# Performance work log

Measured on AMD Instinct MI355X. Metric: run time of the kernel, lower is better.

Reference implementation:

```python
import jax, jax.numpy as jnp
import numpy as np

# ---- module config (mirrors arch_args / init_kwargs) ----
W_BITS_PER_SLICE = 4      # slice_init=True -> weights quantized with STE to w_bits_per_slice
A_BITS = 8                # activation quantization bits
A_BITS_PER_STREAM = 8
VMAX = 1.0
GON_HW, GOFF_HW = 1.0, 1e-3   # weight_to_diff_conductance is called with Gon=1, Goff=1/1000 (hardcoded)
ADC_PREC = 8
ADC_STEP = 1e-3           # adc_static_step
NUM_SUBARRAYS = 9
SUB_SIZE = 256            # subarray_size; 256*3*3 / 256 = 9 even chunks
K, STRIDE, PAD = 3, 1, 1


def ste_quantize(x, bits):
    # Symmetric uniform quantizer with straight-through estimator (STE_Quantize).
    n = float(2 ** bits - 1)
    s = jnp.max(jnp.abs(x)) + 1e-12
    q = jnp.round(x / s * n) / n * s
    return x + jax.lax.stop_gradient(q - x)


def adc_quantize(I):
    # Nbit_ADC: static-step uniform ADC, signed (adc_pos_only=False), deterministic
    # rounding (adc_stoch_round=False), STE backward, no custom loss.
    half = 2 ** (ADC_PREC - 1)
    q = jnp.clip(jnp.round(I / ADC_STEP), -half, half - 1) * ADC_STEP
    return I + jax.lax.stop_gradient(q - I)


def setup_inputs():
    key = jax.random.key(0)
    k1, k2 = jax.random.split(key)
    x = jax.random.normal(k1, (32, 256, 32, 32), jnp.float32)
    fan_in = 256 * K * K
    w = jax.random.normal(k2, (256, 256, K, K), jnp.float32) * np.sqrt(2.0 / fan_in)  # kaiming_normal
    return {"inputs": x, "weight": w}


def reference(inputs, weight):
    B = inputs.shape[0]
    O = weight.shape[0]

    # forward(): quantize activations (a_bits) and weights (w_bits_per_slice, slice_init path)
    qa = ste_quantize(inputs, A_BITS)
    qw = ste_quantize(weight, W_BITS_PER_SLICE)

    # F.unfold -> [B, C*k*k, L], channel-major patch ordering (matches torch)
    patches = jax.lax.conv_general_dilated_patches(
        qa, (K, K), (STRIDE, STRIDE), ((PAD, PAD), (PAD, PAD)))
    Hp, Wp = patches.shape[2], patches.shape[3]
    L = Hp * Wp
    V = patches.reshape(B, NUM_SUBARRAYS, SUB_SIZE, L) * (VMAX / A_BITS_PER_STREAM)

    # Differential conductances: G_pos - G_neg. The dummy columns (both filled with
    # Goff) cancel exactly in I_pos - I_neg, so the net current per subarray is a
    # single contraction against qw * (Gon - Goff) / Nstates_slice.
    nstates = float(2 ** W_BITS_PER_SLICE - 1)
    Gd = qw.reshape(O, NUM_SUBARRAYS, SUB_SIZE) * ((GON_HW - GOFF_HW) / nstates)

    # per-subarray crossbar currents: [B, n_sub, O, L]
    I = jnp.einsum('bgfl,ogf->bgol', V, Gd)

    # shared ADC applied to each subarray output, then accumulate over subarrays
    accum = adc_quantize(I).sum(axis=1)  # [B, O, L]
    a_loss = jnp.float32(0.0)            # adc_custom_loss=False

    # F.fold with (1,1) kernel onto sqrt(L) x sqrt(L) grid == reshape
    result = accum.reshape(B, O, Hp, Wp)
    return (result, a_loss)
```

## Files before the change

kernel.cpp:

```cpp
#include <hip/hip_runtime.h>
#include <stdint.h>

typedef unsigned short u16;
typedef __attribute__((ext_vector_type(8))) short short8;
typedef __attribute__((ext_vector_type(4))) short s4v;
typedef __attribute__((ext_vector_type(4))) float floatx4;

#define NB 32
#define NC 256
#define NH 32
#define NW 32
#define NO 256
#define NPIX (NH*NW)
#define KPIX 9
#define NG 9
#define RUN 32
#define GK (NG*RUN)
#define KTOT (NG*GK)
#define PADH 34
#define PADSP (PADH*PADH)
#define QA_BSTRIDE (PADSP*NC)
#define CHS 40

#define AS1 __attribute__((address_space(1)))
#define AS3 __attribute__((address_space(3)))

__global__ void fused_pre(const float4* __restrict__ x4, int nx4,
                          const float4* __restrict__ w4, int nw4,
                          float* __restrict__ pmax, u16* __restrict__ qa) {
  int bid = blockIdx.x;
  if (bid >= 1088) {
    int zb = bid - 1088;
    int b = zb / 9;
    int rem = (zb % 9) * 256 + threadIdx.x;
    if (rem >= 2112) return;
    int pb = rem >> 4, c16 = rem & 15;
    int y, x;
    if (pb < 68) { y = (pb >= 34) ? 33 : 0; x = pb % 34; }
    else { int q = pb - 68; y = 1 + (q >> 1); x = (q & 1) ? 33 : 0; }
    uint4 z; z.x = z.y = z.z = z.w = 0u;
    *(uint4*)(qa + ((size_t)(b * PADH + y) * PADH + x) * NC + c16 * 16) = z;
    return;
  }
  const float4* p; int n4; int nb, b0;
  if (bid < 1024) { p = x4; n4 = nx4; nb = 1024; b0 = bid; }
  else            { p = w4; n4 = nw4; nb = 64;   b0 = bid - 1024; }
  float m = 0.f;
  for (int i = b0 * blockDim.x + threadIdx.x; i < n4; i += nb * blockDim.x) {
    float4 v = p[i];
    m = fmaxf(m, fmaxf(fmaxf(fabsf(v.x), fabsf(v.y)), fmaxf(fabsf(v.z), fabsf(v.w))));
  }
#pragma unroll
  for (int off = 32; off > 0; off >>= 1)
    m = fmaxf(m, __shfl_down(m, off, 64));
  __shared__ float sm[4];
  int lane = threadIdx.x & 63, wv = threadIdx.x >> 6;
  if (lane == 0) sm[wv] = m;
  __syncthreads();
  if (threadIdx.x == 0)
    pmax[bid] = fmaxf(fmaxf(sm[0], sm[1]), fmaxf(sm[2], sm[3]));
}

__device__ inline void reduce_pmax(const float* pmax, int tid, int nthreads,
                                   float* sred, float& mx_out, float& mw_out) {
  const float4* pf4 = (const float4*)pmax;
  float mx = 0.f, mw = 0.f;
  for (int t = tid; t < 256; t += nthreads) {
    float4 v = pf4[t];
    mx = fmaxf(mx, fmaxf(fmaxf(v.x, v.y), fmaxf(v.z, v.w)));
  }
  if (tid < 16) {
    float4 v = pf4[256 + tid];
    mw = fmaxf(fmaxf(v.x, v.y), fmaxf(v.z, v.w));
  }
#pragma unroll
  for (int off = 32; off > 0; off >>= 1) {
    mx = fmaxf(mx, __shfl_down(mx, off, 64));
    mw = fmaxf(mw, __shfl_down(mw, off, 64));
  }
  int lane = tid & 63, wv = tid >> 6, nw = nthreads >> 6;
  if (lane == 0) { sred[wv] = mx; sred[8 + wv] = mw; }
  __syncthreads();
  mx = sred[0]; mw = sred[8];
  for (int i = 1; i < nw; i++) { mx = fmaxf(mx, sred[i]); mw = fmaxf(mw, sred[8 + i]); }
  mx_out = mx; mw_out = mw;
}

__global__ void fused_quant(const float* __restrict__ x, const float* __restrict__ w,
                            const float* __restrict__ pmax,
                            u16* __restrict__ qa, u16* __restrict__ wq,
                            float* __restrict__ lossp) {
  __shared__ float sred[16];
  float mx, mw;
  reduce_pmax(pmax, threadIdx.x, 256, sred, mx, mw);
  int bid = blockIdx.x, tid = threadIdx.x;
  if (bid < 1024) {
    __shared__ u16 ts[32][264];
    double s = (double)mx + 1e-12;
    double inv = 255.0 / s;
    int b = bid >> 5, y = bid & 31;
    const float4* x4 = (const float4*)x;
    int xc = tid & 7, crow = tid >> 3;
#pragma unroll
    for (int it = 0; it < 8; it++) {
      int c = crow + 32 * it;
      float4 v = x4[((size_t)(b * NC + c) * NH + y) * 8 + xc];
      float q0 = (float)rint((double)v.x * inv);
      float q1 = (float)rint((double)v.y * inv);
      float q2 = (float)rint((double)v.z * inv);
      float q3 = (float)rint((double)v.w * inv);
      ts[xc * 4 + 0][c] = (u16)(__float_as_uint(q0) >> 16);
      ts[xc * 4 + 1][c] = (u16)(__float_as_uint(q1) >> 16);
      ts[xc * 4 + 2][c] = (u16)(__float_as_uint(q2) >> 16);
      ts[xc * 4 + 3][c] = (u16)(__float_as_uint(q3) >> 16);
    }
    __syncthreads();
    int xx = tid >> 3, qwl = tid & 7;
    u16* orow = qa + ((size_t)(b * PADH + y + 1) * PADH + (xx + 1)) * NC;
#pragma unroll
    for (int it = 0; it < 4; it++) {
      int qw = qwl + 8 * it;
      *(uint4*)(orow + qw * 8) = *(const uint4*)&ts[xx][qw * 8];
    }
    return;
  }
  double s = (double)mw + 1e-12;
  double inv = 15.0 / s;
  int idx = (bid - 1024) * 256 + tid;
  if (idx == 0) *lossp = 0.0f;
  int o = idx / KTOT, kk = idx % KTOT;
  int g = kk / GK, rem = kk % GK;
  int r = rem / RUN, j = rem % RUN;
  int clo = (256 * g - r + 8) / 9;
  int chi = (256 * (g + 1) - r + 8) / 9; if (chi > NC) chi = NC;
  int cst = clo & ~3;
  int c = cst + j;
  float val = 0.f;
  if (c >= clo && c < chi) {
    float wv = w[((size_t)o * NC + c) * KPIX + r];
    val = (float)rint((double)wv * inv);
  }
  wq[idx] = (u16)(__float_as_uint(val) >> 16);
}

__global__ __launch_bounds__(256, 2) void gemm_adc(const u16* __restrict__ qa,
                                                   const u16* __restrict__ wq,
                                                   const float* __restrict__ pmax,
                                                   float* __restrict__ out) {
  __shared__ u16 sA[8192];
  __shared__ u16 lB[3 * 128 * RUN];
  __shared__ float sred[16];
  const int tid = threadIdx.x;
  float mx, mw;
  reduce_pmax(pmax, tid, 256, sred, mx, mw);

  const int mblk = blockIdx.x, nblk = blockIdx.y;
  const int b = mblk >> 3;
  const int p0 = (mblk & 7) * 128;
  const int y0 = (mblk & 7) * 4;
  const int n0 = nblk * 128;
  const int lane = tid & 63, wv = tid >> 6;
  const int wm = (wv & 1) * 64, wn = (wv >> 1) * 64;
  const int fm = lane & 15, fq = lane >> 4;
  const int swz = (fq + ((fm >> 1) & 3)) & 3;
  const int fq8 = fq * 8;

  double sa = (double)mx + 1e-12;
  double sw = (double)mw + 1e-12;
  double Sstep = sa * sw * 0.999 / 459.0;

  int pix40[4];
#pragma unroll
  for (int mi = 0; mi < 4; mi++) {
    int pr = wm + mi * 16 + fm;
    pix40[mi] = ((pr >> 5) * 34 + (pr & 31)) * CHS;
  }

  const int r0 = tid >> 2;
  const int jsrc = ((tid & 3) - ((tid >> 3) & 3)) & 3;
  const u16* BbH[2];
#pragma unroll
  for (int h = 0; h < 2; h++)
    BbH[h] = wq + (size_t)(n0 + r0 + 64 * h) * KTOT + jsrc * 8;

  const u16* Abase = qa + (size_t)b * QA_BSTRIDE + (size_t)y0 * PADH * NC;

  floatx4 acc[4][4];
  float tot[4][4][4];
#pragma unroll
  for (int mi = 0; mi < 4; mi++)
#pragma unroll
    for (int ni = 0; ni < 4; ni++)
#pragma unroll
      for (int rr = 0; rr < 4; rr++) { acc[mi][ni][rr] = 0.f; tot[mi][ni][rr] = 0.f; }

#pragma unroll 1
  for (int g = 0; g < NG; g++) {
    int cw = ((256 * g) / 9) & ~3;
#pragma unroll 1
    for (int rc = 0; rc < 3; rc++) {
      int kb[3], dA[3];
#pragma unroll
      for (int ri = 0; ri < 3; ri++) {
        int r = rc * 3 + ri;
        int cst = ((256 * g - r + 8) / 9) & ~3;
        dA[ri] = cst - cw;
        kb[ri] = g * GK + r * RUN;
      }
      if (rc == 0) {
        const u16* src = Abase + cw;
#pragma unroll
        for (int i = 0; i < 4; i++) {
          int s = tid + 256 * i;
          int py = s / 170;
          int rem = s - py * 170;
          int px = rem / 5;
          int j = rem - px * 5;
          __builtin_amdgcn_global_load_lds(
              (const AS1 void*)(src + (py * PADH + px) * NC + j * 8),
              (AS3 void*)&sA[s * 8], 16, 0, 0);
        }
      }
#pragma unroll
      for (int i = 0; i < 6; i++)
        __builtin_amdgcn_global_load_lds(
            (const AS1 void*)(BbH[i & 1] + kb[i >> 1]),
            (AS3 void*)&lB[(tid + 256 * i) * 8], 16, 0, 0);
      __syncthreads();
#pragma unroll
      for (int ri = 0; ri < 3; ri++) {
        short8 afr[4], bfr[4];
        int po = rc * (34 * CHS) + ri * CHS + dA[ri] + fq8;
        if (dA[ri] == 0) {
#pragma unroll
          for (int mi = 0; mi < 4; mi++)
            afr[mi] = *(const short8*)&sA[pix40[mi] + po];
        } else {
#pragma unroll
          for (int mi = 0; mi < 4; mi++) {
            union { short8 v8; s4v v4[2]; } u;
            u.v4[0] = *(const s4v*)&sA[pix40[mi] + po];
            u.v4[1] = *(const s4v*)&sA[pix40[mi] + po + 4];
            afr[mi] = u.v8;
          }
        }
#pragma unroll
        for (int ni = 0; ni < 4; ni++)
          bfr[ni] = *(const short8*)&lB[ri * 4096 + (wn + ni * 16 + fm) * RUN + swz * 8];
#pragma unroll
        for (int mi = 0; mi < 4; mi++)
#pragma unroll
          for (int ni = 0; ni < 4; ni++)
            acc[mi][ni] = __builtin_amdgcn_mfma_f32_16x16x32_bf16(afr[mi], bfr[ni], acc[mi][ni], 0, 0, 0);
      }
      __syncthreads();
    }
#pragma unroll
    for (int mi = 0; mi < 4; mi++)
#pragma unroll
      for (int ni = 0; ni < 4; ni++)
#pragma unroll
        for (int rr = 0; rr < 4; rr++) {
          double d = (double)acc[mi][ni][rr] * Sstep;
          float tf = (float)rint(d);
          tf = fminf(fmaxf(tf, -128.f), 127.f);
          tot[mi][ni][rr] += tf;
          acc[mi][ni][rr] = 0.f;
        }
  }
#pragma unroll
  for (int mi = 0; mi < 4; mi++)
#pragma unroll
    for (int ni = 0; ni < 4; ni++) {
      int o = n0 + wn + ni * 16 + fm;
      int p = p0 + wm + mi * 16 + fq * 4;
      float4 o4;
      o4.x = tot[mi][ni][0] * 1e-3f;
      o4.y = tot[mi][ni][1] * 1e-3f;
      o4.z = tot[mi][ni][2] * 1e-3f;
      o4.w = tot[mi][ni][3] * 1e-3f;
      *(float4*)(out + ((size_t)(b * NO + o)) * NPIX + p) = o4;
    }
}

extern "C" void kernel_launch(void* const* d_in, const int* in_sizes, int n_in,
                              void* d_out, int out_size, void* d_ws, size_t ws_size,
                              hipStream_t stream) {
  const float* x = (const float*)d_in[0];
  const float* w = (const float*)d_in[1];
  float* out = (float*)d_out;

  float* pmax = (float*)d_ws;
  u16* qa = (u16*)((char*)d_ws + 8192);
  u16* wq = (u16*)((char*)d_ws + 8192 + 18939904 + 8192);

  fused_pre<<<1376, 256, 0, stream>>>((const float4*)x, (NB * NC * NH * NW) / 4,
                                      (const float4*)w, (NO * NC * KPIX) / 4,
                                      pmax, qa);
  fused_quant<<<1024 + 2592, 256, 0, stream>>>(x, w, pmax, qa, wq, out + (out_size - 1));
  gemm_adc<<<dim3(256, 2), 256, 0, stream>>>(qa, wq, pmax, out);
}
```

Measured before the change: 154.8 us.

## Double-buffer A slab and B tiles with prefetch, swizzled LDS layout

Restructures the GEMM main loop into a flat 27-step software pipeline. Both the weight tile (lB) and the activation slab (sA32/sA8) are double-buffered, and the next stage's loads are issued before computing on the current one. Partial vmcnt waits and raw s_barrier replace full __syncthreads so that global-to-LDS copies overlap the MFMA work. The activation slab moves to a 32-channel rotated (swizzled) layout plus a small 8-channel tail buffer to reduce LDS bank conflicts, and s_setprio is raised around the compute. LDS use roughly doubles, which may reduce occupancy below two blocks per CU, and the hand-counted waitcnts are fragile.

Result: no change. 156.6 us (+1.1%).

```diff
diff --git a/kernel.cpp b/kernel.cpp
--- a/kernel.cpp
+++ b/kernel.cpp
@@ -20,7 +20,6 @@
 #define PADH 34
 #define PADSP (PADH*PADH)
 #define QA_BSTRIDE (PADSP*NC)
-#define CHS 40
 
 #define AS1 __attribute__((address_space(1)))
 #define AS3 __attribute__((address_space(3)))
@@ -147,8 +146,9 @@
                                                    const u16* __restrict__ wq,
                                                    const float* __restrict__ pmax,
                                                    float* __restrict__ out) {
-  __shared__ u16 sA[8192];
-  __shared__ u16 lB[3 * 128 * RUN];
+  __shared__ __align__(16) u16 lB[24576];
+  __shared__ __align__(16) u16 sA32[13056];
+  __shared__ __align__(16) u16 sA8[1632];
   __shared__ float sred[16];
   const int tid = threadIdx.x;
   float mx, mw;
@@ -163,17 +163,16 @@
   const int wm = (wv & 1) * 64, wn = (wv >> 1) * 64;
   const int fm = lane & 15, fq = lane >> 4;
   const int swz = (fq + ((fm >> 1) & 3)) & 3;
-  const int fq8 = fq * 8;
 
   double sa = (double)mx + 1e-12;
   double sw = (double)mw + 1e-12;
   double Sstep = sa * sw * 0.999 / 459.0;
 
-  int pix40[4];
+  int pixb[4];
 #pragma unroll
   for (int mi = 0; mi < 4; mi++) {
     int pr = wm + mi * 16 + fm;
-    pix40[mi] = ((pr >> 5) * 34 + (pr & 31)) * CHS;
+    pixb[mi] = (pr >> 5) * 34 + (pr & 31);
   }
 
   const int r0 = tid >> 2;
@@ -194,67 +193,33 @@
 #pragma unroll
       for (int rr = 0; rr < 4; rr++) { acc[mi][ni][rr] = 0.f; tot[mi][ni][rr] = 0.f; }
 
-#pragma unroll 1
-  for (int g = 0; g < NG; g++) {
-    int cw = ((256 * g) / 9) & ~3;
-#pragma unroll 1
-    for (int rc = 0; rc < 3; rc++) {
-      int kb[3], dA[3];
-#pragma unroll
-      for (int ri = 0; ri < 3; ri++) {
-        int r = rc * 3 + ri;
-        int cst = ((256 * g - r + 8) / 9) & ~3;
-        dA[ri] = cst - cw;
-        kb[ri] = g * GK + r * RUN;
+  auto STAGE_B = [&](int gs, int rcs, int bB) {
+    int kb0 = gs * GK + rcs * 3 * RUN;
+#pragma unroll
+    for (int i = 0; i < 6; i++)
+      __builtin_amdgcn_global_load_lds(
+          (const AS1 void*)(BbH[i & 1] + kb0 + (i >> 1) * RUN),
+          (AS3 void*)&lB[bB + (tid + 256 * i) * 8], 16, 0, 0);
+  };
+  auto STAGE_SLAB = [&](int gp, int aB) {
+    int cw = ((256 * gp) / 9) & ~3;
+    const u16* src = Abase + cw;
+    if (tid < 204) {
+#pragma unroll
+      for (int i = 0; i < 4; i++) {
+        int s = i * 204 + tid;
+        int p = s >> 2;
+        int js = ((s & 3) - ((s >> 3) & 3)) & 3;
+        __builtin_amdgcn_global_load_lds(
+            (const AS1 void*)(src + p * NC + js * 8),
+            (AS3 void*)&sA32[aB + s * 8], 16, 0, 0);
       }
-      if (rc == 0) {
-        const u16* src = Abase + cw;
-#pragma unroll
-        for (int i = 0; i < 4; i++) {
-          int s = tid + 256 * i;
-          int py = s / 170;
-          int rem = s - py * 170;
-          int px = rem / 5;
-          int j = rem - px * 5;
-          __builtin_amdgcn_global_load_lds(
-              (const AS1 void*)(src + (py * PADH + px) * NC + j * 8),
-              (AS3 void*)&sA[s * 8], 16, 0, 0);
-        }
-      }
-#pragma unroll
-      for (int i = 0; i < 6; i++)
-        __builtin_amdgcn_global_load_lds(
-            (const AS1 void*)(BbH[i & 1] + kb[i >> 1]),
-            (AS3 void*)&lB[(tid + 256 * i) * 8], 16, 0, 0);
-      __syncthreads();
-#pragma unroll
-      for (int ri = 0; ri < 3; ri++) {
-        short8 afr[4], bfr[4];
-        int po = rc * (34 * CHS) + ri * CHS + dA[ri] + fq8;
-        if (dA[ri] == 0) {
-#pragma unroll
-          for (int mi = 0; mi < 4; mi++)
-            afr[mi] = *(const short8*)&sA[pix40[mi] + po];
-        } else {
-#pragma unroll
-          for (int mi = 0; mi < 4; mi++) {
-            union { short8 v8; s4v v4[2]; } u;
-            u.v4[0] = *(const s4v*)&sA[pix40[mi] + po];
-            u.v4[1] = *(const s4v*)&sA[pix40[mi] + po + 4];
-            afr[mi] = u.v8;
-          }
-        }
-#pragma unroll
-        for (int ni = 0; ni < 4; ni++)
-          bfr[ni] = *(const short8*)&lB[ri * 4096 + (wn + ni * 16 + fm) * RUN + swz * 8];
-#pragma unroll
-        for (int mi = 0; mi < 4; mi++)
-#pragma unroll
-          for (int ni = 0; ni < 4; ni++)
-            acc[mi][ni] = __builtin_amdgcn_mfma_f32_16x16x32_bf16(afr[mi], bfr[ni], acc[mi][ni], 0, 0, 0);
-      }
-      __syncthreads();
-    }
+      __builtin_amdgcn_global_load_lds(
+          (const AS1 void*)(src + tid * NC + 32),
+          (AS3 void*)&sA8[tid * 8], 16, 0, 0);
+    }
+  };
+  auto FOLD = [&]() {
 #pragma unroll
     for (int mi = 0; mi < 4; mi++)
 #pragma unroll
@@ -267,13 +232,81 @@
           tot[mi][ni][rr] += tf;
           acc[mi][ni][rr] = 0.f;
         }
-  }
+  };
+
+  STAGE_SLAB(0, 0);
+  STAGE_B(0, 0, 0);
+  int gs = 0, rcs = 1;
+  int g = 0, rc = 0, rc3 = 0, rc34 = 0;
+
+#pragma unroll 1
+  for (int t = 0; t < 27; ++t) {
+    const int bb = (t & 1) * 12288;
+    const int ab = (g & 1) * 6528;
+    if (t < 26) {
+      STAGE_B(gs, rcs, ((t + 1) & 1) * 12288);
+      if (++rcs == 3) { rcs = 0; ++gs; }
+    }
+    bool slab_staged = false;
+    if (rc == 2 && g < 8) {
+      STAGE_SLAB(g + 1, ((g + 1) & 1) * 6528);
+      slab_staged = true;
+    }
+    if (rc == 0 && t > 0) FOLD();
+    if (t == 26)           asm volatile("s_waitcnt vmcnt(0)" ::: "memory");
+    else if (slab_staged)  asm volatile("s_waitcnt vmcnt(11)" ::: "memory");
+    else                   asm volatile("s_waitcnt vmcnt(6)" ::: "memory");
+    __builtin_amdgcn_s_barrier();
+    __builtin_amdgcn_sched_barrier(0);
+    __builtin_amdgcn_s_setprio(1);
+#pragma unroll
+    for (int ri = 0; ri < 3; ri++) {
+      int r = rc3 + ri;
+      bool d4 = (g == 7 && r == 0) || (g == 8 && r <= 4);
+      short8 afr[4], bfr[4];
+#pragma unroll
+      for (int ni = 0; ni < 4; ni++)
+        bfr[ni] = *(const short8*)&lB[bb + ri * 4096 + (wn + ni * 16 + fm) * RUN + swz * 8];
+      if (!d4) {
+#pragma unroll
+        for (int mi = 0; mi < 4; mi++) {
+          int P = pixb[mi] + rc34 + ri;
+          int rot = (P >> 1) & 3;
+          afr[mi] = *(const short8*)&sA32[ab + P * 32 + (((fq + rot) & 3) << 3)];
+        }
+      } else {
+#pragma unroll
+        for (int mi = 0; mi < 4; mi++) {
+          int P = pixb[mi] + rc34 + ri;
+          int rot = (P >> 1) & 3;
+          union { short8 v8; s4v v4[2]; } u;
+          u.v4[0] = *(const s4v*)&sA32[ab + P * 32 + (((fq + rot) & 3) << 3) + 4];
+          const u16* hi = (fq < 3) ? &sA32[ab + P * 32 + (((fq + 1 + rot) & 3) << 3)]
+                                   : &sA8[P * 8];
+          u.v4[1] = *(const s4v*)hi;
+          afr[mi] = u.v8;
+        }
+      }
+#pragma unroll
+      for (int mi = 0; mi < 4; mi++)
+#pragma unroll
+        for (int ni = 0; ni < 4; ni++)
+          acc[mi][ni] = __builtin_amdgcn_mfma_f32_16x16x32_bf16(afr[mi], bfr[ni], acc[mi][ni], 0, 0, 0);
+    }
+    __builtin_amdgcn_s_setprio(0);
+    __builtin_amdgcn_sched_barrier(0);
+    __builtin_amdgcn_s_barrier();
+    if (++rc == 3) { rc = 0; ++g; rc3 = 0; rc34 = 0; }
+    else { rc3 += 3; rc34 += 34; }
+  }
+  FOLD();
+
 #pragma unroll
   for (int mi = 0; mi < 4; mi++)
 #pragma unroll
     for (int ni = 0; ni < 4; ni++) {
       int o = n0 + wn + ni * 16 + fm;
-      int p = p0 + wm + mi * 16 + fq * 4;
+      int p = p0 + wm + mi * 16 + (lane >> 4) * 4;
       float4 o4;
       o4.x = tot[mi][ni][0] * 1e-3f;
       o4.y = tot[mi][ni][1] * 1e-3f;
```

## Align weight runs to group base and swizzle A tile for single 16B LDS reads

Applied to the files above, without the earlier changes.

Weight packing now places every kernel-offset run at the same group-aligned channel start, so the A operand no longer needs a per-offset shift. The shared A tile drops the 40-channel padded layout for a 32-channel XOR-swizzled one, which lets each fragment be one 16-byte LDS read from precomputed addresses. The split half-vector reads go away. The r-chunk loop is fully unrolled, the ADC requantisation of the previous group is moved to sit behind the next group's loads, and the next B chunk's load is issued right after each barrier. The cost is more registers for the address table (36 ints per thread), and only 204 threads take part in the A staging.

After: 146.8 us. 1.06x faster.

```diff
diff --git a/kernel.cpp b/kernel.cpp
--- a/kernel.cpp
+++ b/kernel.cpp
@@ -3,7 +3,6 @@
 
 typedef unsigned short u16;
 typedef __attribute__((ext_vector_type(8))) short short8;
-typedef __attribute__((ext_vector_type(4))) short s4v;
 typedef __attribute__((ext_vector_type(4))) float floatx4;
 
 #define NB 32
@@ -20,7 +19,6 @@
 #define PADH 34
 #define PADSP (PADH*PADH)
 #define QA_BSTRIDE (PADSP*NC)
-#define CHS 40
 
 #define AS1 __attribute__((address_space(1)))
 #define AS3 __attribute__((address_space(3)))
@@ -133,7 +131,7 @@
   int r = rem / RUN, j = rem % RUN;
   int clo = (256 * g - r + 8) / 9;
   int chi = (256 * (g + 1) - r + 8) / 9; if (chi > NC) chi = NC;
-  int cst = clo & ~3;
+  int cst = ((256 * g) / 9) & ~3;
   int c = cst + j;
   float val = 0.f;
   if (c >= clo && c < chi) {
@@ -147,8 +145,8 @@
                                                    const u16* __restrict__ wq,
                                                    const float* __restrict__ pmax,
                                                    float* __restrict__ out) {
-  __shared__ u16 sA[8192];
-  __shared__ u16 lB[3 * 128 * RUN];
+  __shared__ __align__(16) u16 lB[12288];
+  __shared__ __align__(16) u16 sA[6528];
   __shared__ float sred[16];
   const int tid = threadIdx.x;
   float mx, mw;
@@ -163,18 +161,26 @@
   const int wm = (wv & 1) * 64, wn = (wv >> 1) * 64;
   const int fm = lane & 15, fq = lane >> 4;
   const int swz = (fq + ((fm >> 1) & 3)) & 3;
-  const int fq8 = fq * 8;
 
   double sa = (double)mx + 1e-12;
   double sw = (double)mw + 1e-12;
   double Sstep = sa * sw * 0.999 / 459.0;
 
-  int pix40[4];
+  const int OFS[9] = {0, 1, 2, 34, 35, 36, 68, 69, 70};
+  int addrA[4][9];
 #pragma unroll
   for (int mi = 0; mi < 4; mi++) {
     int pr = wm + mi * 16 + fm;
-    pix40[mi] = ((pr >> 5) * 34 + (pr & 31)) * CHS;
-  }
+    int pixb = (pr >> 5) * 34 + (pr & 31);
+#pragma unroll
+    for (int t = 0; t < 9; t++) {
+      int P = pixb + OFS[t];
+      addrA[mi][t] = P * 32 + (((fq + ((P >> 1) & 3)) & 3) << 3);
+    }
+  }
+  int bno[4];
+#pragma unroll
+  for (int ni = 0; ni < 4; ni++) bno[ni] = (wn + ni * 16 + fm) * RUN + swz * 8;
 
   const int r0 = tid >> 2;
   const int jsrc = ((tid & 3) - ((tid >> 3) & 3)) & 3;
@@ -184,6 +190,14 @@
     BbH[h] = wq + (size_t)(n0 + r0 + 64 * h) * KTOT + jsrc * 8;
 
   const u16* Abase = qa + (size_t)b * QA_BSTRIDE + (size_t)y0 * PADH * NC;
+  const bool sact = tid < 204;
+  int soff[4], sdst[4];
+#pragma unroll
+  for (int i = 0; i < 4; i++) {
+    int s = i * 204 + tid;
+    soff[i] = (s >> 2) * NC + ((((s & 3) - ((s >> 3) & 3)) & 3) << 3);
+    sdst[i] = s * 8;
+  }
 
   floatx4 acc[4][4];
   float tot[4][4][4];
@@ -197,56 +211,46 @@
 #pragma unroll 1
   for (int g = 0; g < NG; g++) {
     int cw = ((256 * g) / 9) & ~3;
-#pragma unroll 1
+    if (sact) {
+      const u16* srcg = Abase + cw;
+#pragma unroll
+      for (int i = 0; i < 4; i++)
+        __builtin_amdgcn_global_load_lds((const AS1 void*)(srcg + soff[i]),
+                                         (AS3 void*)&sA[sdst[i]], 16, 0, 0);
+    }
+    {
+      int kb0 = g * GK;
+#pragma unroll
+      for (int i = 0; i < 6; i++)
+        __builtin_amdgcn_global_load_lds((const AS1 void*)(BbH[i & 1] + kb0 + (i >> 1) * RUN),
+                                         (AS3 void*)&lB[(tid + 256 * i) * 8], 16, 0, 0);
+    }
+    if (g > 0) {
+#pragma unroll
+      for (int mi = 0; mi < 4; mi++)
+#pragma unroll
+        for (int ni = 0; ni < 4; ni++)
+#pragma unroll
+          for (int rr = 0; rr < 4; rr++) {
+            double d = (double)acc[mi][ni][rr] * Sstep;
+            float tf = (float)rint(d);
+            tf = fminf(fmaxf(tf, -128.f), 127.f);
+            tot[mi][ni][rr] += tf;
+            acc[mi][ni][rr] = 0.f;
+          }
+    }
+#pragma unroll
     for (int rc = 0; rc < 3; rc++) {
-      int kb[3], dA[3];
-#pragma unroll
-      for (int ri = 0; ri < 3; ri++) {
-        int r = rc * 3 + ri;
-        int cst = ((256 * g - r + 8) / 9) & ~3;
-        dA[ri] = cst - cw;
-        kb[ri] = g * GK + r * RUN;
-      }
-      if (rc == 0) {
-        const u16* src = Abase + cw;
-#pragma unroll
-        for (int i = 0; i < 4; i++) {
-          int s = tid + 256 * i;
-          int py = s / 170;
-          int rem = s - py * 170;
-          int px = rem / 5;
-          int j = rem - px * 5;
-          __builtin_amdgcn_global_load_lds(
-              (const AS1 void*)(src + (py * PADH + px) * NC + j * 8),
-              (AS3 void*)&sA[s * 8], 16, 0, 0);
-        }
-      }
-#pragma unroll
-      for (int i = 0; i < 6; i++)
-        __builtin_amdgcn_global_load_lds(
-            (const AS1 void*)(BbH[i & 1] + kb[i >> 1]),
-            (AS3 void*)&lB[(tid + 256 * i) * 8], 16, 0, 0);
       __syncthreads();
 #pragma unroll
       for (int ri = 0; ri < 3; ri++) {
         short8 afr[4], bfr[4];
-        int po = rc * (34 * CHS) + ri * CHS + dA[ri] + fq8;
-        if (dA[ri] == 0) {
-#pragma unroll
-          for (int mi = 0; mi < 4; mi++)
-            afr[mi] = *(const short8*)&sA[pix40[mi] + po];
-        } else {
-#pragma unroll
-          for (int mi = 0; mi < 4; mi++) {
-            union { short8 v8; s4v v4[2]; } u;
-            u.v4[0] = *(const s4v*)&sA[pix40[mi] + po];
-            u.v4[1] = *(const s4v*)&sA[pix40[mi] + po + 4];
-            afr[mi] = u.v8;
-          }
-        }
+#pragma unroll
+        for (int mi = 0; mi < 4; mi++)
+          afr[mi] = *(const short8*)&sA[addrA[mi][rc * 3 + ri]];
 #pragma unroll
         for (int ni = 0; ni < 4; ni++)
-          bfr[ni] = *(const short8*)&lB[ri * 4096 + (wn + ni * 16 + fm) * RUN + swz * 8];
+          bfr[ni] = *(const short8*)&lB[ri * 4096 + bno[ni]];
 #pragma unroll
         for (int mi = 0; mi < 4; mi++)
 #pragma unroll
@@ -254,20 +258,27 @@
             acc[mi][ni] = __builtin_amdgcn_mfma_f32_16x16x32_bf16(afr[mi], bfr[ni], acc[mi][ni], 0, 0, 0);
       }
       __syncthreads();
-    }
-#pragma unroll
-    for (int mi = 0; mi < 4; mi++)
-#pragma unroll
-      for (int ni = 0; ni < 4; ni++)
-#pragma unroll
-        for (int rr = 0; rr < 4; rr++) {
-          double d = (double)acc[mi][ni][rr] * Sstep;
-          float tf = (float)rint(d);
-          tf = fminf(fmaxf(tf, -128.f), 127.f);
-          tot[mi][ni][rr] += tf;
-          acc[mi][ni][rr] = 0.f;
-        }
-  }
+      if (rc < 2) {
+        int kb0 = g * GK + (rc + 1) * 3 * RUN;
+#pragma unroll
+        for (int i = 0; i < 6; i++)
+          __builtin_amdgcn_global_load_lds((const AS1 void*)(BbH[i & 1] + kb0 + (i >> 1) * RUN),
+                                           (AS3 void*)&lB[(tid + 256 * i) * 8], 16, 0, 0);
+      }
+    }
+  }
+#pragma unroll
+  for (int mi = 0; mi < 4; mi++)
+#pragma unroll
+    for (int ni = 0; ni < 4; ni++)
+#pragma unroll
+      for (int rr = 0; rr < 4; rr++) {
+        double d = (double)acc[mi][ni][rr] * Sstep;
+        float tf = (float)rint(d);
+        tf = fminf(fmaxf(tf, -128.f), 127.f);
+        tot[mi][ni][rr] += tf;
+      }
+
 #pragma unroll
   for (int mi = 0; mi < 4; mi++)
 #pragma unroll
```
